# Kernel tuning notes

Hardware: AMD Instinct MI355X
Metric: run time of the kernel (lower is better)

## Reference

```python
import jax, jax.numpy as jnp
import numpy as np

B, C, H, W = 2, 64, 96, 96
CI = C // 2  # inter_channels


def _conv1x1(x, w, b):
    # x: (B,C,H,W), w: (O,C), b: (O,) -> (B,O,H,W)
    return jnp.einsum('bchw,oc->bohw', x, w) + b[None, :, None, None]


def setup_inputs() -> dict:
    key = jax.random.key(0)
    ks = jax.random.split(key, 9)
    s_in = 1.0 / np.sqrt(C)
    s_ci = 1.0 / np.sqrt(CI)
    return {
        'x': jax.random.normal(ks[0], (B, C, H, W), jnp.float32),
        'theta_w': jax.random.uniform(ks[1], (CI, C), jnp.float32, -s_in, s_in),
        'theta_b': jax.random.uniform(ks[2], (CI,), jnp.float32, -s_in, s_in),
        'phi_w': jax.random.uniform(ks[3], (CI, C), jnp.float32, -s_in, s_in),
        'phi_b': jax.random.uniform(ks[4], (CI,), jnp.float32, -s_in, s_in),
        'g_w': jax.random.uniform(ks[5], (CI, C), jnp.float32, -s_in, s_in),
        'g_b': jax.random.uniform(ks[6], (CI,), jnp.float32, -s_in, s_in),
        'rec_w': jax.random.uniform(ks[7], (C, CI), jnp.float32, -s_ci, s_ci),
        'rec_b': jax.random.uniform(ks[8], (C,), jnp.float32, -s_ci, s_ci),
    }


def reference(x, theta_w, theta_b, phi_w, phi_b, g_w, g_b, rec_w, rec_b):
    b, c, h, w = x.shape
    n = h * w
    # 1x1 conv projections, flattened to (B, N, CI)
    theta = _conv1x1(x, theta_w, theta_b).reshape(b, CI, n).transpose(0, 2, 1)
    phi = _conv1x1(x, phi_w, phi_b).reshape(b, CI, n)            # (B, CI, N)
    g = _conv1x1(x, g_w, g_b).reshape(b, CI, n).transpose(0, 2, 1)  # (B, N, CI)
    # f = theta @ phi^T / N  (no softmax)
    f = jnp.einsum('bnc,bcm->bnm', theta, phi) / n  # (B, N, N)
    y = jnp.einsum('bnm,bmc->bnc', f, g)            # (B, N, CI)
    y = y.transpose(0, 2, 1).reshape(b, CI, h, w)
    z = x + _conv1x1(y, rec_w, rec_b)
    return z
```

## Files before the change

### kernel.cpp

```cpp
#include <hip/hip_runtime.h>

#define BB 2
#define CC 64
#define CI 32
#define NPIX 9216
#define CH 128
#define NCHK (NPIX / CH)
#define NB (BB * NCHK)

__global__ __launch_bounds__(512) void k1_Mpart(
    const float* __restrict__ x, const float* __restrict__ pw,
    const float* __restrict__ pb, const float* __restrict__ gw,
    const float* __restrict__ gb, float* __restrict__ Mpart) {
  __shared__ float xt[CC][CH + 4];
  __shared__ float pgw[2 * CI][CC + 1];
  __shared__ float Ps[CI][CH + 4];
  __shared__ float Gs[CI][CH + 4];
  const int t = threadIdx.x;
  const int blk = blockIdx.x;
  const int batch = blk / NCHK;
  const int chk = blk - batch * NCHK;
  const float* __restrict__ X = x + (size_t)batch * CC * NPIX + chk * CH;

#pragma unroll
  for (int h = 0; h < 4; ++h) {
    const int idx = t + 512 * h;
    const int c = idx >> 5;
    const int p4 = (idx & 31) * 4;
    *reinterpret_cast<float4*>(&xt[c][p4]) =
        *reinterpret_cast<const float4*>(&X[(size_t)c * NPIX + p4]);
  }
#pragma unroll
  for (int h = 0; h < 4; ++h) {
    const int idx = t + 512 * h;
    const int k = idx >> 6, c = idx & 63;
    pgw[k][c] = pw[idx];
    pgw[CI + k][c] = gw[idx];
  }
  __syncthreads();

  {
    const int k = t & 31;
    const int p0 = (t >> 5) * 8;
    float pa[8] = {};
    float ga[8] = {};
    for (int c = 0; c < CC; ++c) {
      const float4 x0 = *reinterpret_cast<const float4*>(&xt[c][p0]);
      const float4 x1 = *reinterpret_cast<const float4*>(&xt[c][p0 + 4]);
      const float pv = pgw[k][c];
      const float gv = pgw[CI + k][c];
      const float xa[8] = {x0.x, x0.y, x0.z, x0.w, x1.x, x1.y, x1.z, x1.w};
#pragma unroll
      for (int i = 0; i < 8; ++i) {
        pa[i] += pv * xa[i];
        ga[i] += gv * xa[i];
      }
    }
    const float pbk = pb[k];
    const float gbk = gb[k];
    float4 o0, o1;
    o0 = make_float4(pa[0] + pbk, pa[1] + pbk, pa[2] + pbk, pa[3] + pbk);
    o1 = make_float4(pa[4] + pbk, pa[5] + pbk, pa[6] + pbk, pa[7] + pbk);
    *reinterpret_cast<float4*>(&Ps[k][p0]) = o0;
    *reinterpret_cast<float4*>(&Ps[k][p0 + 4]) = o1;
    o0 = make_float4(ga[0] + gbk, ga[1] + gbk, ga[2] + gbk, ga[3] + gbk);
    o1 = make_float4(ga[4] + gbk, ga[5] + gbk, ga[6] + gbk, ga[7] + gbk);
    *reinterpret_cast<float4*>(&Gs[k][p0]) = o0;
    *reinterpret_cast<float4*>(&Gs[k][p0 + 4]) = o1;
  }
  __syncthreads();

  {
    const int kk = t >> 4;
    const int l = t & 15;
    float ma = 0.f, mb = 0.f;
    for (int p4 = 0; p4 < CH; p4 += 4) {
      const float4 pv = *reinterpret_cast<const float4*>(&Ps[kk][p4]);
      const float4 g0 = *reinterpret_cast<const float4*>(&Gs[l][p4]);
      const float4 g1 = *reinterpret_cast<const float4*>(&Gs[l + 16][p4]);
      ma += pv.x * g0.x + pv.y * g0.y + pv.z * g0.z + pv.w * g0.w;
      mb += pv.x * g1.x + pv.y * g1.y + pv.z * g1.z + pv.w * g1.w;
    }
    float* Mp = Mpart + ((size_t)batch * NCHK + chk) * (CI * CI);
    Mp[kk * CI + l] = ma;
    Mp[kk * CI + l + 16] = mb;
  }
}

__global__ __launch_bounds__(512) void k2_apply(
    const float* __restrict__ x, const float* __restrict__ tw,
    const float* __restrict__ tb, const float* __restrict__ rw,
    const float* __restrict__ rb, const float* __restrict__ Mpart,
    float* __restrict__ z) {
  __shared__ float xt[CC][CH + 4];
  __shared__ float Ms[CI][CI + 1];
  __shared__ float T1[CI][CC + 2];
  __shared__ float Wt[CC][CC + 2];
  __shared__ float t2[CI];
  __shared__ float bl[CC];
  const int t = threadIdx.x;
  const int blk = blockIdx.x;
  const int batch = blk / NCHK;
  const int chk = blk - batch * NCHK;

#pragma unroll
  for (int h = 0; h < 4; ++h) {
    const int idx = t + 512 * h;
    const int c = idx >> 5;
    const int p4 = (idx & 31) * 4;
    *reinterpret_cast<float4*>(&xt[c][p4]) = *reinterpret_cast<const float4*>(
        &x[(size_t)batch * CC * NPIX + (size_t)c * NPIX + chk * CH + p4]);
  }

  float4* red = reinterpret_cast<float4*>(&Wt[0][0]);
  {
    const int e = t & 255;
    const int half = t >> 8;
    const float* __restrict__ Mp =
        Mpart + (size_t)batch * NCHK * (CI * CI) + (size_t)e * 4;
    float4 s = make_float4(0.f, 0.f, 0.f, 0.f);
#pragma unroll 4
    for (int k = half * 36; k < half * 36 + 36; ++k) {
      const float4 v =
          *reinterpret_cast<const float4*>(&Mp[(size_t)k * (CI * CI)]);
      s.x += v.x; s.y += v.y; s.z += v.z; s.w += v.w;
    }
    red[half * 256 + e] = s;
  }
  __syncthreads();
  if (t < 256) {
    const float4 a = red[t];
    const float4 b = red[t + 256];
    const int m0 = t * 4;
    Ms[(m0 + 0) >> 5][(m0 + 0) & 31] = a.x + b.x;
    Ms[(m0 + 1) >> 5][(m0 + 1) & 31] = a.y + b.y;
    Ms[(m0 + 2) >> 5][(m0 + 2) & 31] = a.z + b.z;
    Ms[(m0 + 3) >> 5][(m0 + 3) & 31] = a.w + b.w;
  }
  __syncthreads();

  {
    const int j = t & 63;
    const int c0 = (t >> 6) * 4;
#pragma unroll
    for (int cc = 0; cc < 4; ++cc) {
      const int c = c0 + cc;
      float s = 0.f;
      for (int k = 0; k < CI; ++k) s += Ms[k][c] * tw[k * CC + j];
      T1[c][j] = s;
    }
    if (t < CI) {
      float s = 0.f;
      for (int k = 0; k < CI; ++k) s += Ms[k][t] * tb[k];
      t2[t] = s;
    }
  }
  __syncthreads();

  {
    const float invN = 1.0f / (float)NPIX;
    const int j = t & 63;
    const int o0 = (t >> 6) * 8;
#pragma unroll
    for (int oo = 0; oo < 8; ++oo) {
      const int o = o0 + oo;
      float s = 0.f;
      for (int c = 0; c < CI; ++c) s += rw[o * CI + c] * T1[c][j];
      Wt[j][o] = s * invN;
    }
    if (t < CC) {
      float s = 0.f;
      for (int c = 0; c < CI; ++c) s += rw[t * CI + c] * t2[c];
      bl[t] = s * invN + rb[t];
    }
  }
  __syncthreads();

  {
    const int n0 = chk * CH;
    float* __restrict__ Z = z + (size_t)batch * CC * NPIX;
    const int c0 = (t >> 6) * 8;
    const int m0 = (t & 63) * 2;
    float acc[8][2] = {};
#pragma unroll 8
    for (int k = 0; k < CC; ++k) {
      const float2 xv = *reinterpret_cast<const float2*>(&xt[k][m0]);
      const float4 w0 = *reinterpret_cast<const float4*>(&Wt[k][c0]);
      const float4 w1 = *reinterpret_cast<const float4*>(&Wt[k][c0 + 4]);
      const float wa[8] = {w0.x, w0.y, w0.z, w0.w, w1.x, w1.y, w1.z, w1.w};
#pragma unroll
      for (int cc = 0; cc < 8; ++cc) {
        acc[cc][0] += wa[cc] * xv.x;
        acc[cc][1] += wa[cc] * xv.y;
      }
    }
#pragma unroll
    for (int cc = 0; cc < 8; ++cc) {
      const int c = c0 + cc;
      const float2 xr = *reinterpret_cast<const float2*>(&xt[c][m0]);
      const float bb2 = bl[c];
      float2 o;
      o.x = acc[cc][0] + xr.x + bb2;
      o.y = acc[cc][1] + xr.y + bb2;
      *reinterpret_cast<float2*>(&Z[(size_t)c * NPIX + n0 + m0]) = o;
    }
  }
}

extern "C" void kernel_launch(void* const* d_in, const int* in_sizes, int n_in,
                              void* d_out, int out_size, void* d_ws,
                              size_t ws_size, hipStream_t stream) {
  (void)in_sizes; (void)n_in; (void)out_size; (void)ws_size;
  const float* x  = (const float*)d_in[0];
  const float* tw = (const float*)d_in[1];
  const float* tb = (const float*)d_in[2];
  const float* pw = (const float*)d_in[3];
  const float* pb = (const float*)d_in[4];
  const float* gw = (const float*)d_in[5];
  const float* gb = (const float*)d_in[6];
  const float* rw = (const float*)d_in[7];
  const float* rb = (const float*)d_in[8];
  float* z = (float*)d_out;

  float* Mpart = (float*)d_ws;

  hipLaunchKernelGGL(k1_Mpart, dim3(NB), dim3(512), 0, stream,
                     x, pw, pb, gw, gb, Mpart);
  hipLaunchKernelGGL(k2_apply, dim3(NB), dim3(512), 0, stream,
                     x, tw, tb, rw, rb, Mpart, z);
}
```

Baseline: 29.22 us.

## Fuse two kernels into one persistent kernel with a global atomic barrier

Merges the partial-M kernel and the apply kernel into a single launch. Blocks publish their packed 32x32 partials with relaxed atomic stores, then wait at a grid-wide spin barrier on an atomic counter before reducing and applying. This keeps the x tile in shared memory, so it is not reloaded, and removes one kernel launch gap. It adds a memset launch and depends on all 144 blocks being co-resident. The relaxed ordering around the barrier, with no fences, risks reading stale partials.

```diff
diff --git a/kernel.cpp b/kernel.cpp
--- a/kernel.cpp
+++ b/kernel.cpp
@@ -7,15 +7,38 @@
 #define CH 128
 #define NCHK (NPIX / CH)
 #define NB (BB * NCHK)
-
-__global__ __launch_bounds__(512) void k1_Mpart(
-    const float* __restrict__ x, const float* __restrict__ pw,
+#define SLOT_U64 (CI * CI / 2)
+
+static __device__ __forceinline__ unsigned long long pack2(float a, float b) {
+  return ((unsigned long long)__float_as_uint(b) << 32) |
+         (unsigned long long)__float_as_uint(a);
+}
+
+struct Phase2 {
+  float Ms[CI][CI + 1];
+  float T1[CI][CC + 2];
+  float Wt[CC][CC + 2];
+  float t2[CI];
+  float bl[CC];
+};
+struct Phase1 {
+  float pgw[2 * CI][CC + 1];
+  float Ps[CI][CH + 4];
+  float Gs[CI][CH + 4];
+};
+struct Smem {
+  float xt[CC][CH + 4];
+  union { Phase1 p1; Phase2 p2; float2 red[2 * SLOT_U64]; } u;
+};
+
+__global__ __launch_bounds__(512) void fused_nonlocal(
+    const float* __restrict__ x, const float* __restrict__ tw,
+    const float* __restrict__ tb, const float* __restrict__ pw,
     const float* __restrict__ pb, const float* __restrict__ gw,
-    const float* __restrict__ gb, float* __restrict__ Mpart) {
-  __shared__ float xt[CC][CH + 4];
-  __shared__ float pgw[2 * CI][CC + 1];
-  __shared__ float Ps[CI][CH + 4];
-  __shared__ float Gs[CI][CH + 4];
+    const float* __restrict__ gb, const float* __restrict__ rw,
+    const float* __restrict__ rb, float* __restrict__ z,
+    unsigned long long* __restrict__ Mpart, unsigned int* __restrict__ ctr) {
+  __shared__ __align__(16) Smem sm;
   const int t = threadIdx.x;
   const int blk = blockIdx.x;
   const int batch = blk / NCHK;
@@ -27,15 +50,15 @@
     const int idx = t + 512 * h;
     const int c = idx >> 5;
     const int p4 = (idx & 31) * 4;
-    *reinterpret_cast<float4*>(&xt[c][p4]) =
+    *reinterpret_cast<float4*>(&sm.xt[c][p4]) =
         *reinterpret_cast<const float4*>(&X[(size_t)c * NPIX + p4]);
   }
 #pragma unroll
   for (int h = 0; h < 4; ++h) {
     const int idx = t + 512 * h;
     const int k = idx >> 6, c = idx & 63;
-    pgw[k][c] = pw[idx];
-    pgw[CI + k][c] = gw[idx];
+    sm.u.p1.pgw[k][c] = pw[idx];
+    sm.u.p1.pgw[CI + k][c] = gw[idx];
   }
   __syncthreads();
 
@@ -45,10 +68,10 @@
     float pa[8] = {};
     float ga[8] = {};
     for (int c = 0; c < CC; ++c) {
-      const float4 x0 = *reinterpret_cast<const float4*>(&xt[c][p0]);
-      const float4 x1 = *reinterpret_cast<const float4*>(&xt[c][p0 + 4]);
-      const float pv = pgw[k][c];
-      const float gv = pgw[CI + k][c];
+      const float4 x0 = *reinterpret_cast<const float4*>(&sm.xt[c][p0]);
+      const float4 x1 = *reinterpret_cast<const float4*>(&sm.xt[c][p0 + 4]);
+      const float pv = sm.u.p1.pgw[k][c];
+      const float gv = sm.u.p1.pgw[CI + k][c];
       const float xa[8] = {x0.x, x0.y, x0.z, x0.w, x1.x, x1.y, x1.z, x1.w};
 #pragma unroll
       for (int i = 0; i < 8; ++i) {
@@ -58,15 +81,14 @@
     }
     const float pbk = pb[k];
     const float gbk = gb[k];
-    float4 o0, o1;
-    o0 = make_float4(pa[0] + pbk, pa[1] + pbk, pa[2] + pbk, pa[3] + pbk);
-    o1 = make_float4(pa[4] + pbk, pa[5] + pbk, pa[6] + pbk, pa[7] + pbk);
-    *reinterpret_cast<float4*>(&Ps[k][p0]) = o0;
-    *reinterpret_cast<float4*>(&Ps[k][p0 + 4]) = o1;
+    float4 o0 = make_float4(pa[0] + pbk, pa[1] + pbk, pa[2] + pbk, pa[3] + pbk);
+    float4 o1 = make_float4(pa[4] + pbk, pa[5] + pbk, pa[6] + pbk, pa[7] + pbk);
+    *reinterpret_cast<float4*>(&sm.u.p1.Ps[k][p0]) = o0;
+    *reinterpret_cast<float4*>(&sm.u.p1.Ps[k][p0 + 4]) = o1;
     o0 = make_float4(ga[0] + gbk, ga[1] + gbk, ga[2] + gbk, ga[3] + gbk);
     o1 = make_float4(ga[4] + gbk, ga[5] + gbk, ga[6] + gbk, ga[7] + gbk);
-    *reinterpret_cast<float4*>(&Gs[k][p0]) = o0;
-    *reinterpret_cast<float4*>(&Gs[k][p0 + 4]) = o1;
+    *reinterpret_cast<float4*>(&sm.u.p1.Gs[k][p0]) = o0;
+    *reinterpret_cast<float4*>(&sm.u.p1.Gs[k][p0 + 4]) = o1;
   }
   __syncthreads();
 
@@ -75,67 +97,62 @@
     const int l = t & 15;
     float ma = 0.f, mb = 0.f;
     for (int p4 = 0; p4 < CH; p4 += 4) {
-      const float4 pv = *reinterpret_cast<const float4*>(&Ps[kk][p4]);
-      const float4 g0 = *reinterpret_cast<const float4*>(&Gs[l][p4]);
-      const float4 g1 = *reinterpret_cast<const float4*>(&Gs[l + 16][p4]);
+      const float4 pv = *reinterpret_cast<const float4*>(&sm.u.p1.Ps[kk][p4]);
+      const float4 g0 = *reinterpret_cast<const float4*>(&sm.u.p1.Gs[l][p4]);
+      const float4 g1 =
+          *reinterpret_cast<const float4*>(&sm.u.p1.Gs[l + 16][p4]);
       ma += pv.x * g0.x + pv.y * g0.y + pv.z * g0.z + pv.w * g0.w;
       mb += pv.x * g1.x + pv.y * g1.y + pv.z * g1.z + pv.w * g1.w;
     }
-    float* Mp = Mpart + ((size_t)batch * NCHK + chk) * (CI * CI);
-    Mp[kk * CI + l] = ma;
-    Mp[kk * CI + l + 16] = mb;
-  }
-}
-
-__global__ __launch_bounds__(512) void k2_apply(
-    const float* __restrict__ x, const float* __restrict__ tw,
-    const float* __restrict__ tb, const float* __restrict__ rw,
-    const float* __restrict__ rb, const float* __restrict__ Mpart,
-    float* __restrict__ z) {
-  __shared__ float xt[CC][CH + 4];
-  __shared__ float Ms[CI][CI + 1];
-  __shared__ float T1[CI][CC + 2];
-  __shared__ float Wt[CC][CC + 2];
-  __shared__ float t2[CI];
-  __shared__ float bl[CC];
-  const int t = threadIdx.x;
-  const int blk = blockIdx.x;
-  const int batch = blk / NCHK;
-  const int chk = blk - batch * NCHK;
-
-#pragma unroll
-  for (int h = 0; h < 4; ++h) {
-    const int idx = t + 512 * h;
-    const int c = idx >> 5;
-    const int p4 = (idx & 31) * 4;
-    *reinterpret_cast<float4*>(&xt[c][p4]) = *reinterpret_cast<const float4*>(
-        &x[(size_t)batch * CC * NPIX + (size_t)c * NPIX + chk * CH + p4]);
-  }
-
-  float4* red = reinterpret_cast<float4*>(&Wt[0][0]);
+    unsigned long long* Mp = Mpart + (size_t)blk * SLOT_U64;
+    __hip_atomic_store(&Mp[kk * 16 + l], pack2(ma, mb), __ATOMIC_RELAXED,
+                       __HIP_MEMORY_SCOPE_AGENT);
+  }
+
+  __syncthreads();
+  if (t == 0) {
+    __hip_atomic_fetch_add(ctr, 1u, __ATOMIC_RELAXED,
+                           __HIP_MEMORY_SCOPE_AGENT);
+    while (__hip_atomic_load(ctr, __ATOMIC_RELAXED,
+                             __HIP_MEMORY_SCOPE_AGENT) < (unsigned)NB) {
+      __builtin_amdgcn_s_sleep(2);
+    }
+  }
+  __syncthreads();
+
   {
     const int e = t & 255;
     const int half = t >> 8;
-    const float* __restrict__ Mp =
-        Mpart + (size_t)batch * NCHK * (CI * CI) + (size_t)e * 4;
-    float4 s = make_float4(0.f, 0.f, 0.f, 0.f);
+    const unsigned long long* __restrict__ Mp =
+        Mpart + (size_t)batch * NCHK * SLOT_U64;
+    float sa0 = 0.f, sb0 = 0.f, sa1 = 0.f, sb1 = 0.f;
 #pragma unroll 4
     for (int k = half * 36; k < half * 36 + 36; ++k) {
-      const float4 v =
-          *reinterpret_cast<const float4*>(&Mp[(size_t)k * (CI * CI)]);
-      s.x += v.x; s.y += v.y; s.z += v.z; s.w += v.w;
-    }
-    red[half * 256 + e] = s;
-  }
-  __syncthreads();
-  if (t < 256) {
-    const float4 a = red[t];
-    const float4 b = red[t + 256];
-    const int m0 = t * 4;
-    Ms[(m0 + 0) >> 5][(m0 + 0) & 31] = a.x + b.x;
-    Ms[(m0 + 1) >> 5][(m0 + 1) & 31] = a.y + b.y;
-    Ms[(m0 + 2) >> 5][(m0 + 2) & 31] = a.z + b.z;
-    Ms[(m0 + 3) >> 5][(m0 + 3) & 31] = a.w + b.w;
+      const unsigned long long v0 = __hip_atomic_load(
+          &Mp[(size_t)k * SLOT_U64 + e], __ATOMIC_RELAXED,
+          __HIP_MEMORY_SCOPE_AGENT);
+      const unsigned long long v1 = __hip_atomic_load(
+          &Mp[(size_t)k * SLOT_U64 + 256 + e], __ATOMIC_RELAXED,
+          __HIP_MEMORY_SCOPE_AGENT);
+      sa0 += __uint_as_float((unsigned)v0);
+      sb0 += __uint_as_float((unsigned)(v0 >> 32));
+      sa1 += __uint_as_float((unsigned)v1);
+      sb1 += __uint_as_float((unsigned)(v1 >> 32));
+    }
+    sm.u.red[half * 512 + e] = make_float2(sa0, sb0);
+    sm.u.red[half * 512 + 256 + e] = make_float2(sa1, sb1);
+  }
+  __syncthreads();
+  {
+    const float2 a = sm.u.red[t];
+    const float2 b = sm.u.red[512 + t];
+    const int kk = t >> 4;
+    const int l = t & 15;
+    const float msa = a.x + b.x;
+    const float msb = a.y + b.y;
+    __syncthreads();
+    sm.u.p2.Ms[kk][l] = msa;
+    sm.u.p2.Ms[kk][l + 16] = msb;
   }
   __syncthreads();
 
@@ -146,13 +163,13 @@
     for (int cc = 0; cc < 4; ++cc) {
       const int c = c0 + cc;
       float s = 0.f;
-      for (int k = 0; k < CI; ++k) s += Ms[k][c] * tw[k * CC + j];
-      T1[c][j] = s;
+      for (int k = 0; k < CI; ++k) s += sm.u.p2.Ms[k][c] * tw[k * CC + j];
+      sm.u.p2.T1[c][j] = s;
     }
     if (t < CI) {
       float s = 0.f;
-      for (int k = 0; k < CI; ++k) s += Ms[k][t] * tb[k];
-      t2[t] = s;
+      for (int k = 0; k < CI; ++k) s += sm.u.p2.Ms[k][t] * tb[k];
+      sm.u.p2.t2[t] = s;
     }
   }
   __syncthreads();
@@ -165,13 +182,13 @@
     for (int oo = 0; oo < 8; ++oo) {
       const int o = o0 + oo;
       float s = 0.f;
-      for (int c = 0; c < CI; ++c) s += rw[o * CI + c] * T1[c][j];
-      Wt[j][o] = s * invN;
+      for (int c = 0; c < CI; ++c) s += rw[o * CI + c] * sm.u.p2.T1[c][j];
+      sm.u.p2.Wt[j][o] = s * invN;
     }
     if (t < CC) {
       float s = 0.f;
-      for (int c = 0; c < CI; ++c) s += rw[t * CI + c] * t2[c];
-      bl[t] = s * invN + rb[t];
+      for (int c = 0; c < CI; ++c) s += rw[t * CI + c] * sm.u.p2.t2[c];
+      sm.u.p2.bl[t] = s * invN + rb[t];
     }
   }
   __syncthreads();
@@ -184,9 +201,10 @@
     float acc[8][2] = {};
 #pragma unroll 8
     for (int k = 0; k < CC; ++k) {
-      const float2 xv = *reinterpret_cast<const float2*>(&xt[k][m0]);
-      const float4 w0 = *reinterpret_cast<const float4*>(&Wt[k][c0]);
-      const float4 w1 = *reinterpret_cast<const float4*>(&Wt[k][c0 + 4]);
+      const float2 xv = *reinterpret_cast<const float2*>(&sm.xt[k][m0]);
+      const float4 w0 = *reinterpret_cast<const float4*>(&sm.u.p2.Wt[k][c0]);
+      const float4 w1 =
+          *reinterpret_cast<const float4*>(&sm.u.p2.Wt[k][c0 + 4]);
       const float wa[8] = {w0.x, w0.y, w0.z, w0.w, w1.x, w1.y, w1.z, w1.w};
 #pragma unroll
       for (int cc = 0; cc < 8; ++cc) {
@@ -197,8 +215,8 @@
 #pragma unroll
     for (int cc = 0; cc < 8; ++cc) {
       const int c = c0 + cc;
-      const float2 xr = *reinterpret_cast<const float2*>(&xt[c][m0]);
-      const float bb2 = bl[c];
+      const float2 xr = *reinterpret_cast<const float2*>(&sm.xt[c][m0]);
+      const float bb2 = sm.u.p2.bl[c];
       float2 o;
       o.x = acc[cc][0] + xr.x + bb2;
       o.y = acc[cc][1] + xr.y + bb2;
@@ -222,10 +240,10 @@
   const float* rb = (const float*)d_in[8];
   float* z = (float*)d_out;
 
-  float* Mpart = (float*)d_ws;
-
-  hipLaunchKernelGGL(k1_Mpart, dim3(NB), dim3(512), 0, stream,
-                     x, pw, pb, gw, gb, Mpart);
-  hipLaunchKernelGGL(k2_apply, dim3(NB), dim3(512), 0, stream,
-                     x, tw, tb, rw, rb, Mpart, z);
+  unsigned long long* Mpart = (unsigned long long*)d_ws;
+  unsigned int* ctr = (unsigned int*)(Mpart + (size_t)NB * SLOT_U64);
+
+  hipMemsetAsync(ctr, 0, sizeof(unsigned int), stream);
+  hipLaunchKernelGGL(fused_nonlocal, dim3(NB), dim3(512), 0, stream,
+                     x, tw, tb, pw, pb, gw, gb, rw, rb, z, Mpart, ctr);
 }
```

After: 35.60 us. +21.8%, slower.
